# Kernel optimization log

Hardware: AMD Instinct MI355X
Metric: run time of the kernel (lower is better)

## Reference

```python
import jax, jax.numpy as jnp
import numpy as np

B, L, D = 4, 4096, 1024
DFF = 4 * D
CAPACITY = 0.5
K = int(L * CAPACITY)  # 2048 tokens kept per sequence


def setup_inputs() -> dict:
    key = jax.random.key(0)
    ks = jax.random.split(key, 6)
    s = 0.02
    return {
        "x": jax.random.normal(ks[0], (B, L, D), dtype=jnp.float32),
        "W1": jax.random.normal(ks[1], (D, DFF), dtype=jnp.float32) * s,
        "b1": jnp.zeros((DFF,), dtype=jnp.float32),
        "W2": jax.random.normal(ks[2], (DFF, D), dtype=jnp.float32) * s,
        "b2": jnp.zeros((D,), dtype=jnp.float32),
        "wr": jax.random.normal(ks[3], (D,), dtype=jnp.float32) * s,
        "br": jnp.zeros((), dtype=jnp.float32),
    }


def reference(x, W1, b1, W2, b2, wr, br):
    # Router logits: Linear(D, 1) -> [B, L]
    scores = jnp.einsum("bld,d->bl", x, wr) + br
    # Hard top-k token selection (capacity_ratio * L tokens), sorted as in torch
    _, idx = jax.lax.top_k(scores, K)          # [B, K]
    idx = jnp.sort(idx, axis=1)
    # Gather selected tokens
    x_sel = jnp.take_along_axis(x, idx[:, :, None], axis=1)  # [B, K, D]
    # Inner MLP on the gathered subset (standard FFN: D -> 4D GELU -> D)
    h = jax.nn.gelu(jnp.einsum("bkd,df->bkf", x_sel, W1) + b1)
    y_sel = jnp.einsum("bkf,fd->bkd", h, W2) + b2            # [B, K, D]
    # Scatter back into a zero tensor of the full shape
    out = jnp.zeros_like(x)
    out = out.at[jnp.arange(B)[:, None], idx].set(y_sel)
    return out
```

## Files before the change

### kernel.cpp

```cpp
#include <hip/hip_runtime.h>
#include <hip/hip_bf16.h>

#define B_   4
#define L_   4096
#define D_   1024
#define DFF_ 4096
#define K_   2048

typedef __attribute__((ext_vector_type(8))) short bf16x8;
typedef __attribute__((ext_vector_type(4))) float f32x4;
typedef unsigned short u16;

__device__ __forceinline__ u16 f2bf(float f) {
    unsigned u = __float_as_uint(f);
    u += 0x7fffu + ((u >> 16) & 1u);
    return (u16)(u >> 16);
}

__device__ __forceinline__ float gelu_fast(float v) {
    float z = 1.5957691216057308f * v * (1.0f + 0.044715f * v * v);
    float e = __builtin_amdgcn_exp2f(-1.4426950408889634f * z);
    return v * __builtin_amdgcn_rcpf(1.0f + e);
}

__device__ __forceinline__ void gload_lds16(const void* g, void* l) {
    __builtin_amdgcn_global_load_lds(
        (const __attribute__((address_space(1))) void*)g,
        (__attribute__((address_space(3))) void*)l, 16, 0, 0);
}

template<int N> __device__ __forceinline__ void wait_vm() {
    if constexpr (N == 0) asm volatile("s_waitcnt vmcnt(0)" ::: "memory");
    else if constexpr (N == 3) asm volatile("s_waitcnt vmcnt(3)" ::: "memory");
    else if constexpr (N == 4) asm volatile("s_waitcnt vmcnt(4)" ::: "memory");
    __builtin_amdgcn_sched_barrier(0);
}

__global__ __launch_bounds__(256) void prep_kernel(
    const float* __restrict__ x, const float* __restrict__ wr,
    const float* __restrict__ br, float* __restrict__ scores,
    const float* __restrict__ W1, const float* __restrict__ W2,
    u16* __restrict__ W1T, u16* __restrict__ W2T)
{
    __shared__ float t[32][33];
    const int bb = blockIdx.x;
    if (bb < 4096) {
        int gtid  = bb * 256 + threadIdx.x;
        int token = gtid >> 6;
        int lane  = threadIdx.x & 63;
        const float* xr = x + (size_t)token * D_;
        double acc = 0.0;
        #pragma unroll
        for (int i = 0; i < 4; ++i) {
            int off = (lane + i * 64) * 4;
            float4 xv = *(const float4*)(xr + off);
            float4 wv = *(const float4*)(wr + off);
            acc += (double)xv.x * wv.x + (double)xv.y * wv.y +
                   (double)xv.z * wv.z + (double)xv.w * wv.w;
        }
        #pragma unroll
        for (int off = 32; off > 0; off >>= 1)
            acc += __shfl_down(acc, off);
        if (lane == 0) scores[token] = (float)(acc + (double)br[0]);
        return;
    }
    const float* in; u16* outb; int RK, RN, bx, by;
    if (bb < 8192) {
        int i = bb - 4096; in = W1; outb = W1T; RK = D_; RN = DFF_;
        bx = i & 127; by = i >> 7;
    } else {
        int i = bb - 8192; in = W2; outb = W2T; RK = DFF_; RN = D_;
        bx = i & 31; by = i >> 5;
    }
    int n0 = bx * 32, k0 = by * 32;
    int tx = threadIdx.x & 31, ty = threadIdx.x >> 5;
    #pragma unroll
    for (int i = 0; i < 4; ++i)
        t[ty + 8 * i][tx] = in[(size_t)(k0 + ty + 8 * i) * RN + (n0 + tx)];
    __syncthreads();
    #pragma unroll
    for (int i = 0; i < 4; ++i)
        outb[(size_t)(n0 + ty + 8 * i) * RK + (k0 + tx)] = f2bf(t[tx][ty + 8 * i]);
}

__global__ __launch_bounds__(256) void rank_zero_kernel(
    const float* __restrict__ scores, int* __restrict__ sel,
    float* __restrict__ out)
{
    __shared__ float sc[L_];
    __shared__ int selLds[64];
    const int b = blockIdx.y;
    const int t = threadIdx.x;
    const float* sb = scores + b * L_;
    for (int i = t; i < L_; i += 256) sc[i] = sb[i];
    __syncthreads();
    const int tg  = t >> 2;
    const int sub = t & 3;
    const int l   = blockIdx.x * 64 + tg;
    const float s = sc[l];
    int cnt = 0;
    const float4* sc4 = (const float4*)sc;
    const int base4 = sub * 256;
    for (int j4 = 0; j4 < 256; ++j4) {
        float4 v = sc4[base4 + j4];
        int j = (base4 + j4) * 4;
        cnt += (int)((v.x > s) || (v.x == s && (j + 0) < l));
        cnt += (int)((v.y > s) || (v.y == s && (j + 1) < l));
        cnt += (int)((v.z > s) || (v.z == s && (j + 2) < l));
        cnt += (int)((v.w > s) || (v.w == s && (j + 3) < l));
    }
    cnt += __shfl_xor(cnt, 1);
    cnt += __shfl_xor(cnt, 2);
    const int issel = (cnt < K_) ? 1 : 0;
    if (sub == 0) { sel[b * L_ + l] = issel; selLds[tg] = issel; }
    __syncthreads();
    float* obase = out + ((size_t)b * L_ + (size_t)blockIdx.x * 64) * D_;
    const float4 z = make_float4(0.f, 0.f, 0.f, 0.f);
    for (int r = 0; r < 64; ++r)
        if (!selLds[r])
            *(float4*)(obase + (size_t)r * D_ + t * 4) = z;
}

__global__ __launch_bounds__(256) void compact_kernel(
    const int* __restrict__ sel, int* __restrict__ idx)
{
    __shared__ int psum[256];
    int b = blockIdx.x, t = threadIdx.x;
    const int* sb = sel + b * L_;
    int base = t * 16;
    int flags[16]; int c = 0;
    #pragma unroll
    for (int i = 0; i < 16; ++i) { flags[i] = sb[base + i]; c += flags[i]; }
    psum[t] = c;
    __syncthreads();
    if (t == 0) {
        int acc = 0;
        for (int j = 0; j < 256; ++j) { int v = psum[j]; psum[j] = acc; acc += v; }
    }
    __syncthreads();
    int p = psum[t];
    #pragma unroll
    for (int i = 0; i < 16; ++i)
        if (flags[i]) idx[b * K_ + (p++)] = base + i;
}

__global__ __launch_bounds__(256) void gather_bf16_kernel(
    const float* __restrict__ x, const int* __restrict__ idxg,
    int row0, u16* __restrict__ xsel)
{
    int rl = blockIdx.x;
    int grow = row0 + rl;
    int tok = idxg[grow];
    int bb = grow >> 11;
    const float* src = x + ((size_t)bb * L_ + (size_t)tok) * D_;
    int t = threadIdx.x;
    float4 v = *(const float4*)(src + t * 4);
    ushort4 o;
    o.x = f2bf(v.x); o.y = f2bf(v.y); o.z = f2bf(v.z); o.w = f2bf(v.w);
    *(ushort4*)(xsel + (size_t)rl * D_ + t * 4) = o;
}

template<int BM, int KD, int EPI>
__global__ __launch_bounds__(512, 2) void gemm_8ph_kernel(
    const u16* __restrict__ A, const u16* __restrict__ Bm,
    const float* __restrict__ bias, u16* __restrict__ hout,
    float* __restrict__ outp, const int* __restrict__ idxg, int row0)
{
    constexpr int BN     = 256;
    constexpr int NT     = KD / 64;
    constexpr int M_REP  = BM / 32;
    constexpr int M_HALF = BM / 64;
    constexpr int IFL    = BM / 128 + 2;

    __shared__ u16 SH[(BM + BN) * 128];
    u16* SA = SH;
    u16* SB = SH + BM * 128;

    const int tid  = threadIdx.x;
    const int lane = tid & 63;
    const int wid  = tid >> 6;
    const int wm = wid >> 2, wn = wid & 3;
    const int fr = lane & 15;
    const int kq = (lane >> 4) * 8;
    const int rq = (lane >> 4) * 4;

    constexpr int gx = (EPI == 0 ? DFF_ : D_) / 256;
    const int nwg = gridDim.x;
    const int o   = blockIdx.x;
    const int swz = (o & 7) * (nwg >> 3) + (o >> 3);
    const int bn  = (swz % gx) * 256;
    const int bm  = (swz / gx) * BM;

    const int srow = tid >> 2;
    const int skof = (tid & 3) * 8;
    const u16* Abase = A  + (size_t)(bm + srow) * KD + skof;
    const u16* Bbase = Bm + (size_t)(bn + srow) * KD + skof;

    f32x4 acc[M_REP][4];
    #pragma unroll
    for (int m = 0; m < M_REP; ++m)
        #pragma unroll
        for (int n = 0; n < 4; ++n) acc[m][n] = (f32x4)0.0f;

    auto stage = [&](int s) {
        int kt = s >> 2, j = s & 3;
        int d = kt & 1, h = j >> 1;
        int koff = kt * 64 + h * 32;
        if (j & 1) {
            u16* dst = SB + (d * 2 + h) * (BN * 32) + tid * 8;
            gload_lds16(Bbase + koff, dst);
            gload_lds16(Bbase + koff + (size_t)128 * KD, dst + 4096);
        } else {
            u16* dst = SA + (d * 2 + h) * (BM * 32) + tid * 8;
            gload_lds16(Abase + koff, dst);
            if constexpr (BM == 256)
                gload_lds16(Abase + koff + (size_t)128 * KD, dst + 4096);
        }
    };

    #pragma unroll
    for (int s = 0; s < 6; ++s) stage(s);
    wait_vm<IFL>();
    __builtin_amdgcn_s_barrier();

    bf16x8 bfv[4];
    for (int i = 0; i < NT / 2; ++i) {
        #pragma unroll
        for (int p = 0; p < 8; ++p) {
            const int d   = (2 * i + (p >> 2)) & 1;
            const int kh  = (p >> 1) & 1;
            const int mlo = (p & 1) * M_HALF;
            if ((p & 1) == 0) {
                #pragma unroll
                for (int n = 0; n < 4; ++n)
                    bfv[n] = *(const bf16x8*)(SB + (d * 2 + kh) * (BN * 32) +
                              (wn * 64 + n * 16 + fr) * 32 + kq);
            }
            bf16x8 af[M_HALF];
            #pragma unroll
            for (int q = 0; q < M_HALF; ++q)
                af[q] = *(const bf16x8*)(SA + (d * 2 + kh) * (BM * 32) +
                          (wm * (BM / 2) + (mlo + q) * 16 + fr) * 32 + kq);
            int s = 8 * i + p + 6;
            if (s < 4 * NT) stage(s);
            __builtin_amdgcn_s_barrier();
            asm volatile("s_waitcnt lgkmcnt(0)" ::: "memory");
            __builtin_amdgcn_sched_barrier(0);
            __builtin_amdgcn_s_setprio(1);
            #pragma unroll
            for (int q = 0; q < M_HALF; ++q)
                #pragma unroll
                for (int n = 0; n < 4; ++n)
                    acc[mlo + q][n] = __builtin_amdgcn_mfma_f32_16x16x32_bf16(
                        af[q], bfv[n], acc[mlo + q][n], 0, 0, 0);
            __builtin_amdgcn_s_setprio(0);
            if (p == 3) {
                if (i == NT / 2 - 1) wait_vm<0>(); else wait_vm<IFL>();
            } else if (p == 7) {
                if (i < NT / 2 - 1) wait_vm<IFL>();
            }
            __builtin_amdgcn_s_barrier();
        }
    }

    if constexpr (EPI == 0) {
        u16* ct = SH;
        #pragma unroll
        for (int n = 0; n < 4; ++n) {
            const int col = wn * 64 + n * 16 + fr;
            const float bc = bias[bn + col];
            #pragma unroll
            for (int m = 0; m < M_REP; ++m) {
                const int rb = wm * (BM / 2) + m * 16 + rq;
                #pragma unroll
                for (int r = 0; r < 4; ++r) {
                    int row = rb + r;
                    int pc  = col ^ (((row >> 2) & 3) << 4);
                    ct[row * 256 + pc] = f2bf(gelu_fast(acc[m][n][r] + bc));
                }
            }
        }
        __syncthreads();
        const int chunk = tid & 31;
        const int rw    = tid >> 5;
        #pragma unroll
        for (int pass = 0; pass < 16; ++pass) {
            int row = pass * 16 + rw;
            int pb  = (chunk * 8) ^ (((row >> 2) & 3) << 4);
            bf16x8 v = *(const bf16x8*)(ct + row * 256 + pb);
            *(bf16x8*)(hout + (size_t)(bm + row) * DFF_ + bn + chunk * 8) = v;
        }
    } else {
        #pragma unroll
        for (int n = 0; n < 4; ++n) {
            const int col = bn + wn * 64 + n * 16 + fr;
            const float bc = bias[col];
            #pragma unroll
            for (int m = 0; m < M_REP; ++m) {
                const int rbase = bm + wm * (BM / 2) + m * 16 + rq;
                #pragma unroll
                for (int r = 0; r < 4; ++r) {
                    int grow = row0 + rbase + r;
                    int bb = grow >> 11;
                    int tok = idxg[grow];
                    outp[((size_t)bb * L_ + (size_t)tok) * D_ + col] =
                        acc[m][n][r] + bc;
                }
            }
        }
    }
}

extern "C" void kernel_launch(void* const* d_in, const int* in_sizes, int n_in,
                              void* d_out, int out_size, void* d_ws, size_t ws_size,
                              hipStream_t stream)
{
    const float* x  = (const float*)d_in[0];
    const float* W1 = (const float*)d_in[1];
    const float* b1 = (const float*)d_in[2];
    const float* W2 = (const float*)d_in[3];
    const float* b2 = (const float*)d_in[4];
    const float* wr = (const float*)d_in[5];
    const float* br = (const float*)d_in[6];
    float* out = (float*)d_out;

    char* ws = (char*)d_ws;
    int*   idx    = (int*)ws;
    float* scores = (float*)(ws + (32 << 10));
    int*   sel    = (int*)(ws + (96 << 10));
    u16* W1T = (u16*)(ws + (256 << 10));
    u16* W2T = W1T + (size_t)DFF_ * D_;

    size_t fixedB = (size_t)(256 << 10) + (size_t)DFF_ * D_ * 2 * 2;
    size_t avail  = ws_size > fixedB ? ws_size - fixedB : 0;
    int RC = (int)(avail / (size_t)(D_ * 2 + DFF_ * 2));
    RC = (RC / 256) * 256;
    if (RC > B_ * K_) RC = B_ * K_;
    if (RC < 256) RC = 256;
    u16* xsel = (u16*)(ws + fixedB);
    u16* hbuf = xsel + (size_t)RC * D_;

    prep_kernel<<<dim3(12288), 256, 0, stream>>>(x, wr, br, scores, W1, W2, W1T, W2T);
    rank_zero_kernel<<<dim3(L_ / 64, B_), 256, 0, stream>>>(scores, sel, out);
    compact_kernel<<<dim3(B_), 256, 0, stream>>>(sel, idx);

    for (int r0 = 0; r0 < B_ * K_; r0 += RC) {
        int rc = (B_ * K_ - r0 < RC) ? (B_ * K_ - r0) : RC;
        gather_bf16_kernel<<<dim3(rc), 256, 0, stream>>>(x, idx, r0, xsel);
        gemm_8ph_kernel<256, D_, 0><<<dim3((DFF_ / 256) * (rc / 256)), 512, 0, stream>>>(
            xsel, W1T, b1, hbuf, nullptr, nullptr, 0);
        gemm_8ph_kernel<128, DFF_, 1><<<dim3((D_ / 256) * (rc / 128)), 512, 0, stream>>>(
            hbuf, W2T, b2, nullptr, out, idx, r0);
    }
}
```

Before: 221.5 us.

## Reorganize LDS layout to k-chunk-major and use 4-phase pipeline for BM=128

Changes the global-to-LDS staging so each thread loads a row with k-chunk offsets, storing tiles in a chunk-major LDS layout (8-element columns grouped by k-quarter). Fragment reads are adjusted to match, which is meant to reduce LDS bank conflicts on the bf16x8 reads. For BM=128 the 8-phase loop becomes 4 phases with two stage loads per phase, halving barriers per k-tile. The risk is a different global access pattern and pipeline depth tradeoffs.

```diff
diff --git a/kernel.cpp b/kernel.cpp
--- a/kernel.cpp
+++ b/kernel.cpp
@@ -166,11 +166,12 @@
     const float* __restrict__ bias, u16* __restrict__ hout,
     float* __restrict__ outp, const int* __restrict__ idxg, int row0)
 {
-    constexpr int BN     = 256;
-    constexpr int NT     = KD / 64;
-    constexpr int M_REP  = BM / 32;
-    constexpr int M_HALF = BM / 64;
-    constexpr int IFL    = BM / 128 + 2;
+    constexpr int BN    = 256;
+    constexpr int NT    = KD / 64;
+    constexpr int M_REP = BM / 32;
+    constexpr int PH    = (BM == 256) ? 8 : 4;
+    constexpr int SPP   = 8 / PH;
+    constexpr int IFL   = BM / 128 + 2;
 
     __shared__ u16 SH[(BM + BN) * 128];
     u16* SA = SH;
@@ -181,8 +182,8 @@
     const int wid  = tid >> 6;
     const int wm = wid >> 2, wn = wid & 3;
     const int fr = lane & 15;
-    const int kq = (lane >> 4) * 8;
-    const int rq = (lane >> 4) * 4;
+    const int cq = lane >> 4;
+    const int rq = cq * 4;
 
     constexpr int gx = (EPI == 0 ? DFF_ : D_) / 256;
     const int nwg = gridDim.x;
@@ -191,10 +192,10 @@
     const int bn  = (swz % gx) * 256;
     const int bm  = (swz / gx) * BM;
 
-    const int srow = tid >> 2;
-    const int skof = (tid & 3) * 8;
-    const u16* Abase = A  + (size_t)(bm + srow) * KD + skof;
-    const u16* Bbase = Bm + (size_t)(bn + srow) * KD + skof;
+    const int rowA = tid % BM,  cA = tid / BM;
+    const int rowB = tid & 255, cB = tid >> 8;
+    const u16* AbaseS = A  + (size_t)(bm + rowA) * KD + cA * 8;
+    const u16* BbaseS = Bm + (size_t)(bn + rowB) * KD + cB * 8;
 
     f32x4 acc[M_REP][4];
     #pragma unroll
@@ -207,14 +208,14 @@
         int d = kt & 1, h = j >> 1;
         int koff = kt * 64 + h * 32;
         if (j & 1) {
-            u16* dst = SB + (d * 2 + h) * (BN * 32) + tid * 8;
-            gload_lds16(Bbase + koff, dst);
-            gload_lds16(Bbase + koff + (size_t)128 * KD, dst + 4096);
+            u16* dst = SB + (d * 2 + h) * 8192 + tid * 8;
+            gload_lds16(BbaseS + koff, dst);
+            gload_lds16(BbaseS + koff + 16, dst + 4096);
         } else {
             u16* dst = SA + (d * 2 + h) * (BM * 32) + tid * 8;
-            gload_lds16(Abase + koff, dst);
+            gload_lds16(AbaseS + koff, dst);
             if constexpr (BM == 256)
-                gload_lds16(Abase + koff + (size_t)128 * KD, dst + 4096);
+                gload_lds16(AbaseS + koff + 16, dst + 4096);
         }
     };
 
@@ -226,37 +227,42 @@
     bf16x8 bfv[4];
     for (int i = 0; i < NT / 2; ++i) {
         #pragma unroll
-        for (int p = 0; p < 8; ++p) {
-            const int d   = (2 * i + (p >> 2)) & 1;
-            const int kh  = (p >> 1) & 1;
-            const int mlo = (p & 1) * M_HALF;
-            if ((p & 1) == 0) {
+        for (int p = 0; p < PH; ++p) {
+            const int d   = (BM == 256) ? ((p >> 2) & 1) : ((p >> 1) & 1);
+            const int kh  = (BM == 256) ? ((p >> 1) & 1) : (p & 1);
+            const int mlo = (BM == 256) ? (p & 1) * 4 : 0;
+            const bool readB = (BM == 128) || ((p & 1) == 0);
+            const int slot = d * 2 + kh;
+            if (readB) {
                 #pragma unroll
                 for (int n = 0; n < 4; ++n)
-                    bfv[n] = *(const bf16x8*)(SB + (d * 2 + kh) * (BN * 32) +
-                              (wn * 64 + n * 16 + fr) * 32 + kq);
-            }
-            bf16x8 af[M_HALF];
-            #pragma unroll
-            for (int q = 0; q < M_HALF; ++q)
-                af[q] = *(const bf16x8*)(SA + (d * 2 + kh) * (BM * 32) +
-                          (wm * (BM / 2) + (mlo + q) * 16 + fr) * 32 + kq);
-            int s = 8 * i + p + 6;
-            if (s < 4 * NT) stage(s);
+                    bfv[n] = *(const bf16x8*)(SB + slot * 8192 + cq * 2048 +
+                              (wn * 64 + n * 16 + fr) * 8);
+            }
+            bf16x8 af[4];
+            #pragma unroll
+            for (int q = 0; q < 4; ++q)
+                af[q] = *(const bf16x8*)(SA + slot * (BM * 32) + cq * (BM * 8) +
+                          (wm * (BM / 2) + (mlo + q) * 16 + fr) * 8);
+            #pragma unroll
+            for (int u = 0; u < SPP; ++u) {
+                int s = 8 * i + SPP * p + 6 + u;
+                if (s < 4 * NT) stage(s);
+            }
             __builtin_amdgcn_s_barrier();
             asm volatile("s_waitcnt lgkmcnt(0)" ::: "memory");
             __builtin_amdgcn_sched_barrier(0);
             __builtin_amdgcn_s_setprio(1);
             #pragma unroll
-            for (int q = 0; q < M_HALF; ++q)
+            for (int q = 0; q < 4; ++q)
                 #pragma unroll
                 for (int n = 0; n < 4; ++n)
                     acc[mlo + q][n] = __builtin_amdgcn_mfma_f32_16x16x32_bf16(
                         af[q], bfv[n], acc[mlo + q][n], 0, 0, 0);
             __builtin_amdgcn_s_setprio(0);
-            if (p == 3) {
+            if (p == PH / 2 - 1) {
                 if (i == NT / 2 - 1) wait_vm<0>(); else wait_vm<IFL>();
-            } else if (p == 7) {
+            } else if (p == PH - 1) {
                 if (i < NT / 2 - 1) wait_vm<IFL>();
             }
             __builtin_amdgcn_s_barrier();
```

New measurement: 299.1 us. 1.35x slower.
